# Performance work log

Hardware: AMD Instinct MI355X
Metric: run time of the kernel (lower is better)

The kernel has to match this reference:

```python
import jax, jax.numpy as jnp
import numpy as np

B, L, DX, DQ = 8, 4096, 128, 128


def setup_inputs() -> dict:
    key = jax.random.key(0)
    ks = jax.random.split(key, 16)
    g = lambda k, shp, fan: jax.random.normal(k, shp, jnp.float32) * (1.0 / np.sqrt(fan))
    return {
        'x': jax.random.normal(ks[0], (B, L, DX), jnp.float32),
        'c': jax.random.normal(ks[1], (B, DQ), jnp.float32),
        # CrossAttention('add') params (all Linear weights stored as (in, out))
        'W1': g(ks[2], (DX, DX), DX),          # w1, bias frozen at 0
        'W2': g(ks[3], (DQ, DX), DQ),          # w2, bias frozen at 0
        'wt_w': g(ks[4], (DX,), DX),           # wt: dx -> 1, bias frozen at 0
        'bsa': jnp.zeros((DX,), jnp.float32),
        # csa pairwise-score params
        'Wsa1': g(ks[5], (DX, DX), DX),        # bias frozen at 0
        'Wsa2': g(ks[6], (DX, DX), DX),        # bias frozen at 0
        'wsat_w': g(ks[7], (DX,), DX),         # wsat: dx -> 1
        'wsat_b': jnp.zeros((), jnp.float32),
        'bsa1': jnp.zeros((DX,), jnp.float32),
        # PositionwiseFeedForward(dx, dx)
        'pfn_w1': g(ks[8], (DX, DX), DX),
        'pfn_b1': jnp.zeros((DX,), jnp.float32),
        'pfn_w2': g(ks[9], (DX, DX), DX),
        'pfn_b2': jnp.zeros((DX,), jnp.float32),
        'ln_g': jnp.ones((DX,), jnp.float32),
        'ln_b': jnp.zeros((DX,), jnp.float32),
    }


def reference(x, c, W1, W2, wt_w, bsa, Wsa1, Wsa2, wsat_w, wsat_b, bsa1,
              pfn_w1, pfn_b1, pfn_w2, pfn_b2, ln_g, ln_b):
    seq_len = x.shape[-2]
    # ---- CrossAttention, mode='add': p = softmax(wt(w1(x) + w2(c) + bsa), dim=-2) ----
    wx = jnp.einsum('bld,de->ble', x, W1)                 # (B, L, dx)
    wq = jnp.einsum('bd,de->be', c, W2)                   # (B, dx)
    logits = jnp.einsum('ble,e->bl', wx + wq[:, None, :] + bsa, wt_w)
    p = jax.nn.softmax(logits, axis=-1)[..., None]        # softmax over L -> (B, L, 1)
    h = x * p                                             # (B, L, dx)
    # ---- pairwise additive scores: wsat(Wsa1(h)_i + Wsa2(h)_j + bsa1) ----
    # wsat is linear, so the (B,L,L,dx) tensor decomposes exactly into rank-1 terms.
    si = jnp.einsum('ble,e->bl', jnp.einsum('bld,de->ble', h, Wsa1), wsat_w)  # (B, L)
    sj = jnp.einsum('ble,e->bl', jnp.einsum('bld,de->ble', h, Wsa2), wsat_w)  # (B, L)
    const = jnp.dot(bsa1, wsat_w) + wsat_b
    scores = jax.nn.sigmoid(si[:, :, None] + sj[:, None, :] + const)          # (B, L, L)
    # mask diagonal with -inf then softmax over last dim (j)
    diag = jnp.eye(seq_len, dtype=bool)
    scores = jnp.where(diag, -jnp.inf, scores)
    A = jax.nn.softmax(scores, axis=-1)                   # (B, L, L)
    # ui = sum_i A[b,i,j] * x[b,j,:]  (faithful to fcsa * x.unsqueeze(1) summed over dim 1)
    ui = x * jnp.sum(A, axis=1)[..., None]                # (B, L, dx)
    # ---- PositionwiseFeedForward with residual + LayerNorm(eps=1e-6); dropout=eval/identity ----
    y = jnp.maximum(jnp.einsum('bld,de->ble', ui, pfn_w1) + pfn_b1, 0.0)
    y = jnp.einsum('ble,ed->bld', y, pfn_w2) + pfn_b2 + ui
    mu = jnp.mean(y, axis=-1, keepdims=True)
    var = jnp.mean(jnp.square(y - mu), axis=-1, keepdims=True)
    return (y - mu) / jnp.sqrt(var + 1e-6) * ln_g + ln_b
```

## Files before the change

### kernel.cpp

```cpp
#include <hip/hip_runtime.h>


#define SEQ 4096
#define NB 8
#define DXC 128
#define SQRTE 1.6487212707001282f
#define Y1S 136

typedef __attribute__((ext_vector_type(8))) short short8;
typedef __attribute__((ext_vector_type(4))) float f32x4;

__device__ __forceinline__ float wave_sum(float v) {
#pragma unroll
  for (int m = 32; m >= 1; m >>= 1) v += __shfl_xor(v, m);
  return v;
}

__device__ __forceinline__ float qwave_sum(float v) {
#pragma unroll
  for (int m = 8; m >= 1; m >>= 1) v += __shfl_xor(v, m);
  return v;
}

__device__ __forceinline__ unsigned short f2bf(float f) {
  unsigned int u = __float_as_uint(f);
  unsigned int r = (u + 0x7FFFu + ((u >> 16) & 1u)) >> 16;
  return (unsigned short)r;
}

__device__ __forceinline__ float dot128(const float* __restrict__ a,
                                        const float* __restrict__ b) {
  const float4* A = (const float4*)a;
  const float4* B = (const float4*)b;
  float s = 0.f;
#pragma unroll 8
  for (int i = 0; i < 32; ++i) {
    float4 u = A[i], v = B[i];
    s += u.x * v.x + u.y * v.y + u.z * v.z + u.w * v.w;
  }
  return s;
}

__device__ __forceinline__ void get_ck(float* ck) {
  ck[0] = 1.0f;
  ck[1] = 0.25f;
  ck[2] = 0.03125f;
  ck[3] = -7.0f / 384.0f;
  ck[4] = -31.0f / 6144.0f;
  ck[5] = 177.0f / 122880.0f;
  ck[6] = 2017.0f / 2949120.0f;
}

__device__ __forceinline__ float binomf(int k, int m) {
  const float B[7][7] = {
      {1, 0, 0, 0, 0, 0, 0},  {1, 1, 0, 0, 0, 0, 0},   {1, 2, 1, 0, 0, 0, 0},
      {1, 3, 3, 1, 0, 0, 0},  {1, 4, 6, 4, 1, 0, 0},   {1, 5, 10, 10, 5, 1, 0},
      {1, 6, 15, 20, 15, 6, 1}};
  return B[k][m];
}

__device__ __forceinline__ void sep_coeffs(const float* V, float* C) {
  float ck[7];
  get_ck(ck);
#pragma unroll
  for (int m = 0; m < 7; ++m) {
    float acc = 0.f;
    for (int n = 0; n <= 6 - m; ++n) acc += ck[m + n] * binomf(m + n, m) * V[n];
    C[m] = SQRTE * acc;
  }
}

__device__ __forceinline__ float horner7(const float* C, float a) {
  return (((((C[6] * a + C[5]) * a + C[4]) * a + C[3]) * a + C[2]) * a + C[1])
             * a + C[0];
}

__device__ __forceinline__ float g_exact(float t) {
  float sg = 1.0f / (1.0f + __expf(-t));
  return __expf(sg);
}


__global__ __launch_bounds__(256) void prep(
    const float* __restrict__ W1, const float* __restrict__ Wsa1,
    const float* __restrict__ Wsa2, const float* __restrict__ wt_w,
    const float* __restrict__ wsat_w, const float* __restrict__ wsat_b,
    const float* __restrict__ bsa1, const float* __restrict__ pw1,
    const float* __restrict__ pw2, float* __restrict__ ws_f,
    unsigned short* __restrict__ Wt1, unsigned short* __restrict__ Wt2) {
  int blk = blockIdx.x, tid = threadIdx.x;
  if (blk < 32) {
    int e0 = blk * 1024 + tid * 4;
    int which = e0 >> 14;
    int k = e0 & 16383;
    int eo = k >> 7, d0 = k & 127;
    const float* pw = which ? pw2 : pw1;
    unsigned short* Wt = which ? Wt2 : Wt1;
#pragma unroll
    for (int j = 0; j < 4; ++j)
      Wt[eo * DXC + d0 + j] = f2bf(pw[(d0 + j) * DXC + eo]);
  } else if (blk == 32) {
    if (tid < 128) {
      ws_f[128 + tid] = dot128(W1 + tid * DXC, wt_w);
      ws_f[256 + tid] = dot128(Wsa1 + tid * DXC, wsat_w);
      ws_f[384 + tid] = dot128(Wsa2 + tid * DXC, wsat_w);
    } else if (tid == 128) {
      ws_f[512] = dot128(bsa1, wsat_w) + wsat_b[0];
    }
  } else {
    if (tid < 128) ws_f[tid] = 0.f;
  }
}

__global__ __launch_bounds__(256) void rowstats(
    const float* __restrict__ x, const float* __restrict__ ws_f,
    float* __restrict__ ap_g, float* __restrict__ w_g,
    float* __restrict__ acc) {
  __shared__ float vs[3 * DXC];
  __shared__ float t0s[64], t1s[64], t2s[64];
  int tid = threadIdx.x, blk = blockIdx.x;
  int base = blk * 64;
  int b = blk >> 6;
  for (int k = tid; k < 384; k += 256) vs[k] = ws_f[128 + k];
  __syncthreads();
  int lane = tid & 63, wave = tid >> 6;
  int seg = lane & 15, sub = lane >> 4;
  float4 v00 = *(const float4*)&vs[0 * DXC + seg * 8];
  float4 v01 = *(const float4*)&vs[0 * DXC + seg * 8 + 4];
  float4 v10 = *(const float4*)&vs[1 * DXC + seg * 8];
  float4 v11 = *(const float4*)&vs[1 * DXC + seg * 8 + 4];
  float4 v20 = *(const float4*)&vs[2 * DXC + seg * 8];
  float4 v21 = *(const float4*)&vs[2 * DXC + seg * 8 + 4];
  const float* xb = x + (size_t)base * DXC;
#pragma unroll
  for (int p = 0; p < 4; ++p) {
    int rl = wave * 16 + p * 4 + sub;
    const float4* xp = (const float4*)(xb + (size_t)rl * DXC + seg * 8);
    float4 lo = xp[0], hi = xp[1];
    float s0 = lo.x * v00.x + lo.y * v00.y + lo.z * v00.z + lo.w * v00.w
             + hi.x * v01.x + hi.y * v01.y + hi.z * v01.z + hi.w * v01.w;
    float s1 = lo.x * v10.x + lo.y * v10.y + lo.z * v10.z + lo.w * v10.w
             + hi.x * v11.x + hi.y * v11.y + hi.z * v11.z + hi.w * v11.w;
    float s2 = lo.x * v20.x + lo.y * v20.y + lo.z * v20.z + lo.w * v20.w
             + hi.x * v21.x + hi.y * v21.y + hi.z * v21.z + hi.w * v21.w;
    s0 = qwave_sum(s0);
    s1 = qwave_sum(s1);
    s2 = qwave_sum(s2);
    if (seg == 0) { t0s[rl] = s0; t1s[rl] = s1; t2s[rl] = s2; }
  }
  __syncthreads();
  if (tid < 64) {
    float e = __expf(t0s[tid]);
    float w = e * t2s[tid];
    ap_g[base + tid] = e * t1s[tid];
    w_g[base + tid] = w;
    float r[7];
    r[0] = e;
    r[1] = w;
#pragma unroll
    for (int n = 2; n < 7; ++n) r[n] = r[n - 1] * w;
#pragma unroll
    for (int n = 0; n < 7; ++n) r[n] = wave_sum(r[n]);
    if (tid == 0) {
      atomicAdd(&acc[b], r[0]);
#pragma unroll
      for (int n = 1; n < 7; ++n) atomicAdd(&acc[8 + b * 6 + n - 1], r[n]);
    }
  }
}

__global__ __launch_bounds__(256) void zqpass(
    const float* __restrict__ ap_g, const float* __restrict__ w_g,
    const float* __restrict__ ws_f, float* __restrict__ sj_g,
    float* __restrict__ dcol_g, float* __restrict__ acc) {
  __shared__ float red[4][7];
  int tid = threadIdx.x, blk = blockIdx.x;
  int gid = blk * 256 + tid;
  int b = blk >> 4;
  float invS = 1.0f / acc[b];
  float Sv[7], P[7];
  Sv[0] = (float)SEQ;
  float ip = invS;
#pragma unroll
  for (int n = 1; n < 7; ++n) { Sv[n] = acc[8 + b * 6 + n - 1] * ip; ip *= invS; }
  sep_coeffs(Sv, P);
  float ccst = ws_f[512];
  float a = ap_g[gid] * invS + ccst;
  float bb = w_g[gid] * invS;
  float zf = horner7(P, a);
  float d = g_exact(a + bb);
  float iz = 1.0f / (zf - d);
  sj_g[gid] = bb;
  dcol_g[gid] = d * iz;
  float t[7];
  t[0] = iz;
#pragma unroll
  for (int n = 1; n < 7; ++n) t[n] = t[n - 1] * a;
#pragma unroll
  for (int n = 0; n < 7; ++n) t[n] = wave_sum(t[n]);
  int lane = tid & 63, wave = tid >> 6;
  if (lane == 0) {
#pragma unroll
    for (int n = 0; n < 7; ++n) red[wave][n] = t[n];
  }
  __syncthreads();
  if (tid < 7) {
    float s = red[0][tid] + red[1][tid] + red[2][tid] + red[3][tid];
    atomicAdd(&acc[64 + b * 8 + tid], s);
  }
}

__global__ __launch_bounds__(256) void ffn_mfma(
    const float* __restrict__ x, const float* __restrict__ sj_g,
    const float* __restrict__ dcol_g, const float* __restrict__ acc,
    const unsigned short* __restrict__ Wt1,
    const unsigned short* __restrict__ Wt2,
    const float* __restrict__ b1, const float* __restrict__ b2,
    const float* __restrict__ lng, const float* __restrict__ lnb,
    float* __restrict__ out) {
  __shared__ float cs[64];
  __shared__ __align__(16) unsigned short y1[64 * Y1S];
  int tid = threadIdx.x;
  int base = blockIdx.x * 64;
  int b = blockIdx.x >> 6;
  if (tid < 64) {
    float Tv[7], Q[7];
#pragma unroll
    for (int n = 0; n < 7; ++n) Tv[n] = acc[64 + b * 8 + n];
    sep_coeffs(Tv, Q);
    int row = base + tid;
    cs[tid] = horner7(Q, sj_g[row]) - dcol_g[row];
  }
  __syncthreads();
  int lane = tid & 63, wave = tid >> 6;
  int n16 = lane & 15, quad = lane >> 4;
  int m0 = wave * 16;
  int rowA = base + m0 + n16;
  float csA = cs[m0 + n16];
  const float4* xr = (const float4*)(x + (size_t)rowA * DXC);
  short8 afr[4];
#pragma unroll
  for (int cc = 0; cc < 4; ++cc) {
    float4 p0 = xr[cc * 8 + quad * 2];
    float4 p1 = xr[cc * 8 + quad * 2 + 1];
    short8 af;
    af[0] = (short)f2bf(p0.x * csA); af[1] = (short)f2bf(p0.y * csA);
    af[2] = (short)f2bf(p0.z * csA); af[3] = (short)f2bf(p0.w * csA);
    af[4] = (short)f2bf(p1.x * csA); af[5] = (short)f2bf(p1.y * csA);
    af[6] = (short)f2bf(p1.z * csA); af[7] = (short)f2bf(p1.w * csA);
    afr[cc] = af;
  }
#pragma unroll
  for (int nt = 0; nt < 8; ++nt) {
    const unsigned short* wrow = Wt1 + (nt * 16 + n16) * DXC;
    f32x4 a = {0.f, 0.f, 0.f, 0.f};
#pragma unroll
    for (int cc = 0; cc < 4; ++cc) {
      short8 bf = *(const short8*)(wrow + cc * 32 + quad * 8);
      a = __builtin_amdgcn_mfma_f32_16x16x32_bf16(afr[cc], bf, a, 0, 0, 0);
    }
    float b1v = b1[nt * 16 + n16];
#pragma unroll
    for (int r = 0; r < 4; ++r) {
      float yv = fmaxf(a[r] + b1v, 0.f);
      y1[(m0 + quad * 4 + r) * Y1S + nt * 16 + n16] = f2bf(yv);
    }
  }
  __syncthreads();
  const unsigned short* yrow = &y1[(m0 + n16) * Y1S];
  short8 afr2[4];
#pragma unroll
  for (int cc = 0; cc < 4; ++cc)
    afr2[cc] = *(const short8*)(yrow + cc * 32 + quad * 8);
  f32x4 acc2[8];
#pragma unroll
  for (int nt = 0; nt < 8; ++nt) {
    const unsigned short* wrow = Wt2 + (nt * 16 + n16) * DXC;
    f32x4 a = {0.f, 0.f, 0.f, 0.f};
#pragma unroll
    for (int cc = 0; cc < 4; ++cc) {
      short8 bf = *(const short8*)(wrow + cc * 32 + quad * 8);
      a = __builtin_amdgcn_mfma_f32_16x16x32_bf16(afr2[cc], bf, a, 0, 0, 0);
    }
    acc2[nt] = a;
  }
  float b2v[8], lgv[8], lbv[8];
#pragma unroll
  for (int nt = 0; nt < 8; ++nt) {
    int col = nt * 16 + n16;
    b2v[nt] = b2[col]; lgv[nt] = lng[col]; lbv[nt] = lnb[col];
  }
#pragma unroll
  for (int r = 0; r < 4; ++r) {
    int rl = m0 + quad * 4 + r;
    int row = base + rl;
    float csr = cs[rl];
    const float* xrow = x + (size_t)row * DXC;
    float z[8];
    float s = 0.f, sq = 0.f;
#pragma unroll
    for (int nt = 0; nt < 8; ++nt) {
      int col = nt * 16 + n16;
      float zz = acc2[nt][r] + b2v[nt] + xrow[col] * csr;
      z[nt] = zz; s += zz; sq += zz * zz;
    }
#pragma unroll
    for (int mm = 8; mm >= 1; mm >>= 1) {
      s += __shfl_xor(s, mm);
      sq += __shfl_xor(sq, mm);
    }
    float mu = s * 0.0078125f;
    float var = sq * 0.0078125f - mu * mu;
    float rstd = 1.0f / sqrtf(var + 1e-6f);
    float* orow = out + (size_t)row * DXC;
#pragma unroll
    for (int nt = 0; nt < 8; ++nt) {
      int col = nt * 16 + n16;
      orow[col] = (z[nt] - mu) * rstd * lgv[nt] + lbv[nt];
    }
  }
}

extern "C" void kernel_launch(void* const* d_in, const int* in_sizes, int n_in,
                              void* d_out, int out_size, void* d_ws, size_t ws_size,
                              hipStream_t stream) {
  const float* x = (const float*)d_in[0];
  const float* W1 = (const float*)d_in[2];
  const float* wt_w = (const float*)d_in[4];
  const float* Wsa1 = (const float*)d_in[6];
  const float* Wsa2 = (const float*)d_in[7];
  const float* wsat_w = (const float*)d_in[8];
  const float* wsat_b = (const float*)d_in[9];
  const float* bsa1 = (const float*)d_in[10];
  const float* pw1 = (const float*)d_in[11];
  const float* pb1 = (const float*)d_in[12];
  const float* pw2 = (const float*)d_in[13];
  const float* pb2 = (const float*)d_in[14];
  const float* lng = (const float*)d_in[15];
  const float* lnb = (const float*)d_in[16];
  float* out = (float*)d_out;
  float* ws = (float*)d_ws;

  const int NR = NB * SEQ;
  float* acc = ws;
  float* ap_g = ws + 1024;
  float* w_g = ap_g + NR;
  float* sj_g = w_g + NR;
  float* dcol_g = sj_g + NR;
  unsigned short* Wt1 = (unsigned short*)(dcol_g + NR);
  unsigned short* Wt2 = Wt1 + DXC * DXC;

  prep<<<34, 256, 0, stream>>>(W1, Wsa1, Wsa2, wt_w, wsat_w, wsat_b, bsa1,
                               pw1, pw2, ws, Wt1, Wt2);
  rowstats<<<512, 256, 0, stream>>>(x, ws, ap_g, w_g, acc);
  zqpass<<<128, 256, 0, stream>>>(ap_g, w_g, ws, sj_g, dcol_g, acc);
  ffn_mfma<<<512, 256, 0, stream>>>(x, sj_g, dcol_g, acc, Wt1, Wt2, pb1, pb2,
                                    lng, lnb, out);
}
```

Before: 155.5 us.

## Eliminate prep kernel and replace atomics with per-block partial sums

Removes the separate prep launch. Each rowstats block now computes the three projection vectors itself, and zqpass does the weight transpose and bf16 conversion plus the bias constant. The global atomicAdd accumulators are replaced by per-block partial arrays that the next kernel sums, so no zero-initialisation pass is needed. This saves one launch and its serialization, but every rowstats block redundantly computes 384 dot products of length 128 over the weight matrices.

```diff
diff --git a/kernel.cpp b/kernel.cpp
--- a/kernel.cpp
+++ b/kernel.cpp
@@ -80,48 +80,23 @@
   return __expf(sg);
 }
 
-
-__global__ __launch_bounds__(256) void prep(
-    const float* __restrict__ W1, const float* __restrict__ Wsa1,
-    const float* __restrict__ Wsa2, const float* __restrict__ wt_w,
-    const float* __restrict__ wsat_w, const float* __restrict__ wsat_b,
-    const float* __restrict__ bsa1, const float* __restrict__ pw1,
-    const float* __restrict__ pw2, float* __restrict__ ws_f,
-    unsigned short* __restrict__ Wt1, unsigned short* __restrict__ Wt2) {
-  int blk = blockIdx.x, tid = threadIdx.x;
-  if (blk < 32) {
-    int e0 = blk * 1024 + tid * 4;
-    int which = e0 >> 14;
-    int k = e0 & 16383;
-    int eo = k >> 7, d0 = k & 127;
-    const float* pw = which ? pw2 : pw1;
-    unsigned short* Wt = which ? Wt2 : Wt1;
-#pragma unroll
-    for (int j = 0; j < 4; ++j)
-      Wt[eo * DXC + d0 + j] = f2bf(pw[(d0 + j) * DXC + eo]);
-  } else if (blk == 32) {
-    if (tid < 128) {
-      ws_f[128 + tid] = dot128(W1 + tid * DXC, wt_w);
-      ws_f[256 + tid] = dot128(Wsa1 + tid * DXC, wsat_w);
-      ws_f[384 + tid] = dot128(Wsa2 + tid * DXC, wsat_w);
-    } else if (tid == 128) {
-      ws_f[512] = dot128(bsa1, wsat_w) + wsat_b[0];
-    }
-  } else {
-    if (tid < 128) ws_f[tid] = 0.f;
-  }
-}
-
 __global__ __launch_bounds__(256) void rowstats(
-    const float* __restrict__ x, const float* __restrict__ ws_f,
+    const float* __restrict__ x, const float* __restrict__ W1,
+    const float* __restrict__ Wsa1, const float* __restrict__ Wsa2,
+    const float* __restrict__ wt_w, const float* __restrict__ wsat_w,
     float* __restrict__ ap_g, float* __restrict__ w_g,
-    float* __restrict__ acc) {
+    float* __restrict__ part1) {
   __shared__ float vs[3 * DXC];
   __shared__ float t0s[64], t1s[64], t2s[64];
   int tid = threadIdx.x, blk = blockIdx.x;
   int base = blk * 64;
-  int b = blk >> 6;
-  for (int k = tid; k < 384; k += 256) vs[k] = ws_f[128 + k];
+  if (tid < 128) {
+    vs[tid] = dot128(W1 + tid * DXC, wt_w);
+    vs[2 * DXC + tid] = dot128(Wsa2 + tid * DXC, wsat_w);
+  } else {
+    int d = tid - 128;
+    vs[DXC + d] = dot128(Wsa1 + d * DXC, wsat_w);
+  }
   __syncthreads();
   int lane = tid & 63, wave = tid >> 6;
   int seg = lane & 15, sub = lane >> 4;
@@ -162,30 +137,62 @@
 #pragma unroll
     for (int n = 0; n < 7; ++n) r[n] = wave_sum(r[n]);
     if (tid == 0) {
-      atomicAdd(&acc[b], r[0]);
-#pragma unroll
-      for (int n = 1; n < 7; ++n) atomicAdd(&acc[8 + b * 6 + n - 1], r[n]);
+#pragma unroll
+      for (int n = 0; n < 7; ++n) part1[blk * 8 + n] = r[n];
     }
   }
 }
 
 __global__ __launch_bounds__(256) void zqpass(
     const float* __restrict__ ap_g, const float* __restrict__ w_g,
-    const float* __restrict__ ws_f, float* __restrict__ sj_g,
-    float* __restrict__ dcol_g, float* __restrict__ acc) {
+    const float* __restrict__ part1, const float* __restrict__ bsa1,
+    const float* __restrict__ wsat_w, const float* __restrict__ wsat_b,
+    const float* __restrict__ pw1, const float* __restrict__ pw2,
+    float* __restrict__ sj_g, float* __restrict__ dcol_g,
+    float* __restrict__ part2, unsigned short* __restrict__ Wt1,
+    unsigned short* __restrict__ Wt2) {
+  __shared__ float Ss[8];
+  __shared__ float ccst_sh;
   __shared__ float red[4][7];
   int tid = threadIdx.x, blk = blockIdx.x;
   int gid = blk * 256 + tid;
   int b = blk >> 4;
-  float invS = 1.0f / acc[b];
+  {
+    int which = gid >> 14;
+    int k = gid & 16383;
+    int eo = k >> 7, dd = k & 127;
+    const float* pw = which ? pw2 : pw1;
+    unsigned short* Wt = which ? Wt2 : Wt1;
+    Wt[eo * DXC + dd] = f2bf(pw[dd * DXC + eo]);
+  }
+  if (tid < 64) {
+    const float* p = part1 + ((size_t)b * 64 + tid) * 8;
+    float r[7];
+#pragma unroll
+    for (int n = 0; n < 7; ++n) r[n] = p[n];
+#pragma unroll
+    for (int n = 0; n < 7; ++n) r[n] = wave_sum(r[n]);
+    if (tid == 0) {
+#pragma unroll
+      for (int n = 0; n < 7; ++n) Ss[n] = r[n];
+    }
+  }
+  if (tid >= 64 && tid < 128) {
+    int l = tid - 64;
+    float2 bv = ((const float2*)bsa1)[l];
+    float2 wv = ((const float2*)wsat_w)[l];
+    float s = wave_sum(bv.x * wv.x + bv.y * wv.y);
+    if (l == 0) ccst_sh = s + wsat_b[0];
+  }
+  __syncthreads();
+  float invS = 1.0f / Ss[0];
   float Sv[7], P[7];
   Sv[0] = (float)SEQ;
   float ip = invS;
 #pragma unroll
-  for (int n = 1; n < 7; ++n) { Sv[n] = acc[8 + b * 6 + n - 1] * ip; ip *= invS; }
+  for (int n = 1; n < 7; ++n) { Sv[n] = Ss[n] * ip; ip *= invS; }
   sep_coeffs(Sv, P);
-  float ccst = ws_f[512];
-  float a = ap_g[gid] * invS + ccst;
+  float a = ap_g[gid] * invS + ccst_sh;
   float bb = w_g[gid] * invS;
   float zf = horner7(P, a);
   float d = g_exact(a + bb);
@@ -205,28 +212,36 @@
   }
   __syncthreads();
   if (tid < 7) {
-    float s = red[0][tid] + red[1][tid] + red[2][tid] + red[3][tid];
-    atomicAdd(&acc[64 + b * 8 + tid], s);
+    part2[blk * 8 + tid] =
+        red[0][tid] + red[1][tid] + red[2][tid] + red[3][tid];
   }
 }
 
 __global__ __launch_bounds__(256) void ffn_mfma(
     const float* __restrict__ x, const float* __restrict__ sj_g,
-    const float* __restrict__ dcol_g, const float* __restrict__ acc,
+    const float* __restrict__ dcol_g, const float* __restrict__ part2,
     const unsigned short* __restrict__ Wt1,
     const unsigned short* __restrict__ Wt2,
     const float* __restrict__ b1, const float* __restrict__ b2,
     const float* __restrict__ lng, const float* __restrict__ lnb,
     float* __restrict__ out) {
+  __shared__ float Ts[8];
   __shared__ float cs[64];
   __shared__ __align__(16) unsigned short y1[64 * Y1S];
   int tid = threadIdx.x;
   int base = blockIdx.x * 64;
   int b = blockIdx.x >> 6;
+  if (tid < 7) {
+    float s = 0.f;
+#pragma unroll
+    for (int j = 0; j < 16; ++j) s += part2[((size_t)b * 16 + j) * 8 + tid];
+    Ts[tid] = s;
+  }
+  __syncthreads();
   if (tid < 64) {
     float Tv[7], Q[7];
 #pragma unroll
-    for (int n = 0; n < 7; ++n) Tv[n] = acc[64 + b * 8 + n];
+    for (int n = 0; n < 7; ++n) Tv[n] = Ts[n];
     sep_coeffs(Tv, Q);
     int row = base + tid;
     cs[tid] = horner7(Q, sj_g[row]) - dcol_g[row];
@@ -342,18 +357,19 @@
   float* ws = (float*)d_ws;
 
   const int NR = NB * SEQ;
-  float* acc = ws;
-  float* ap_g = ws + 1024;
+  float* part1 = ws;
+  float* part2 = ws + 4096;
+  float* ap_g = ws + 8192;
   float* w_g = ap_g + NR;
   float* sj_g = w_g + NR;
   float* dcol_g = sj_g + NR;
   unsigned short* Wt1 = (unsigned short*)(dcol_g + NR);
   unsigned short* Wt2 = Wt1 + DXC * DXC;
 
-  prep<<<34, 256, 0, stream>>>(W1, Wsa1, Wsa2, wt_w, wsat_w, wsat_b, bsa1,
-                               pw1, pw2, ws, Wt1, Wt2);
-  rowstats<<<512, 256, 0, stream>>>(x, ws, ap_g, w_g, acc);
-  zqpass<<<128, 256, 0, stream>>>(ap_g, w_g, ws, sj_g, dcol_g, acc);
-  ffn_mfma<<<512, 256, 0, stream>>>(x, sj_g, dcol_g, acc, Wt1, Wt2, pb1, pb2,
-                                    lng, lnb, out);
-}
+  rowstats<<<512, 256, 0, stream>>>(x, W1, Wsa1, Wsa2, wt_w, wsat_w, ap_g,
+                                    w_g, part1);
+  zqpass<<<128, 256, 0, stream>>>(ap_g, w_g, part1, bsa1, wsat_w, wsat_b,
+                                  pw1, pw2, sj_g, dcol_g, part2, Wt1, Wt2);
+  ffn_mfma<<<512, 256, 0, stream>>>(x, sj_g, dcol_g, part2, Wt1, Wt2, pb1,
+                                    pb2, lng, lnb, out);
+}
```

Measured after the change: 133.7 us. 14.0% less time.
